# Performance work log

Measured on AMD Instinct MI355X. Metric: run time of the kernel, lower is better.

## Reference

```python
import jax, jax.numpy as jnp
import numpy as np

N, E, D, L = 100000, 600000, 128, 5
BN_EPS = 1e-5


def setup_inputs() -> dict:
    key = jax.random.key(0)
    ks = jax.random.split(key, 12)
    x = jax.random.normal(ks[0], (N, D), dtype=jnp.float32)
    edge_index = jax.random.randint(ks[1], (2, E), 0, N, dtype=jnp.int64)
    edge_attr = jax.random.randint(ks[2], (E, D), 0, 4, dtype=jnp.int32)
    # per-layer GCNConv params
    W = jax.random.normal(ks[3], (L, D, D), dtype=jnp.float32) * 0.05
    b = jax.random.normal(ks[4], (L, D), dtype=jnp.float32) * 0.01
    root = jax.random.normal(ks[5], (L, D), dtype=jnp.float32) * 0.05
    # BatchNorm1d eval-mode params / running stats
    gamma = 1.0 + 0.1 * jax.random.normal(ks[6], (L, D), dtype=jnp.float32)
    beta = 0.1 * jax.random.normal(ks[7], (L, D), dtype=jnp.float32)
    mean = 0.1 * jax.random.normal(ks[8], (L, D), dtype=jnp.float32)
    var = 0.5 + jax.random.uniform(ks[9], (L, D), dtype=jnp.float32)
    return {"x": x, "edge_index": edge_index, "edge_attr": edge_attr,
            "W": W, "b": b, "root": root,
            "gamma": gamma, "beta": beta, "mean": mean, "var": var}


def reference(x, edge_index, edge_attr, W, b, root, gamma, beta, mean, var):
    # edge_attr.long() then identity edge_encoder -> integer values used in float math
    e = edge_attr.astype(x.dtype)                      # [E, D]
    row, col = edge_index[0], edge_index[1]            # source j, target i
    # deg = degree(row) + 1 (same every layer since graph is fixed)
    deg = jax.ops.segment_sum(jnp.ones((E,), x.dtype), row, num_segments=N) + 1.0  # [N]
    dinv = deg ** -0.5
    norm = (dinv[row] * dinv[col])[:, None]            # [E, 1]
    h = x
    for l in range(L):
        hl = h @ W[l].T + b[l]                         # Linear(emb_dim, emb_dim)
        msg = norm * jax.nn.relu(hl[row] + e)          # gather + relu + scale  [E, D]
        agg = jax.ops.segment_sum(msg, col, num_segments=N)  # scatter-add at targets
        h = agg + jax.nn.relu(hl + root[l]) / deg[:, None]   # self-loop term
        # BatchNorm1d (eval mode, running stats)
        h = gamma[l] * (h - mean[l]) / jnp.sqrt(var[l] + BN_EPS) + beta[l]
        if l < L - 1:
            h = jax.nn.relu(h)                         # dropout is identity in eval
    return h  # JK='last'
```

## Files before the change

### kernel.cpp

```cpp
#include <hip/hip_runtime.h>
#include <cstdint>
#include <cstddef>

#define DF 128
#define NL 5
#define NB 1024
#define BN_EPS 1e-5f

typedef short bf16x8 __attribute__((ext_vector_type(8)));
typedef float f32x4 __attribute__((ext_vector_type(4)));

typedef __attribute__((address_space(3))) uint32_t lds_u32;
typedef __attribute__((address_space(1))) uint32_t glb_u32;

__device__ __forceinline__ void gload16(const void* g, void* l) {
#if __has_builtin(__builtin_amdgcn_global_load_lds)
  __builtin_amdgcn_global_load_lds((const glb_u32*)g, (lds_u32*)l, 16, 0, 0);
#else
  *(uint4*)l = *(const uint4*)g;
#endif
}

__device__ __forceinline__ ushort f2b(float f) {
  union { float f; uint32_t u; } v; v.f = f;
  uint32_t u = v.u + 0x7fffu + ((v.u >> 16) & 1u);
  return (ushort)(u >> 16);
}
__device__ __forceinline__ uint32_t pk2(float a, float b) {
  return (uint32_t)f2b(a) | ((uint32_t)f2b(b) << 16);
}
__device__ __forceinline__ float i8f(uint32_t w, int sh) {
  return (float)(int8_t)((w >> sh) & 0xffu);
}


__global__ void k_deg2(const int* __restrict__ row, const int* __restrict__ col,
                       int* __restrict__ degi, int* __restrict__ indeg, int E) {
  int i = blockIdx.x * blockDim.x + threadIdx.x;
  if (i < E) {
    atomicAdd(&degi[row[i]], 1);
    atomicAdd(&indeg[col[i]], 1);
  }
}

__global__ void k_dinvhist(const int* __restrict__ degi, const int* __restrict__ indeg,
                           float* __restrict__ dinv, int* __restrict__ hist, int N) {
  __shared__ int lh[NB];
  for (int j = threadIdx.x; j < NB; j += blockDim.x) lh[j] = 0;
  __syncthreads();
  int i = blockIdx.x * blockDim.x + threadIdx.x;
  if (i < N) {
    dinv[i] = 1.0f / sqrtf((float)(degi[i] + 1));
    atomicAdd(&lh[min(indeg[i], NB - 1)], 1);
  }
  __syncthreads();
  for (int j = threadIdx.x; j < NB; j += blockDim.x) {
    int c = lh[j];
    if (c) atomicAdd(&hist[j], c);
  }
}

__global__ void k_scan(const int* __restrict__ hist,
                       int* __restrict__ nodeStart, int* __restrict__ edgeStart) {
  __shared__ int2 sm[NB];
  int t = threadIdx.x;
  int c = hist[t];
  int2 v; v.x = c; v.y = c * t;
  sm[t] = v;
  __syncthreads();
  for (int off = 1; off < NB; off <<= 1) {
    int2 add; add.x = 0; add.y = 0;
    if (t >= off) add = sm[t - off];
    __syncthreads();
    sm[t].x += add.x; sm[t].y += add.y;
    __syncthreads();
  }
  nodeStart[t] = sm[t].x - c;
  edgeStart[t] = sm[t].y - c * t;
}

__global__ void k_assign(const int* __restrict__ indeg, const float* __restrict__ dinv,
                         const int* __restrict__ nodeStart, const int* __restrict__ edgeStart,
                         int* __restrict__ binCursor,
                         int* __restrict__ perm, int* __restrict__ invperm,
                         int* __restrict__ startP, int* __restrict__ cursorP,
                         int* __restrict__ degP, float* __restrict__ dinvP, int N) {
  __shared__ int lh[NB];
  __shared__ int gbase[NB];
  for (int j = threadIdx.x; j < NB; j += blockDim.x) lh[j] = 0;
  __syncthreads();
  int nd = blockIdx.x * blockDim.x + threadIdx.x;
  bool valid = nd < N;
  int d = 0, bin = 0, lrank = 0;
  if (valid) {
    d = indeg[nd];
    bin = min(d, NB - 1);
    lrank = atomicAdd(&lh[bin], 1);
  }
  __syncthreads();
  for (int j = threadIdx.x; j < NB; j += blockDim.x) {
    int c = lh[j];
    gbase[j] = c ? atomicAdd(&binCursor[j], c) : 0;
  }
  __syncthreads();
  if (!valid) return;
  int r = gbase[bin] + lrank;
  int i = nodeStart[bin] + r;
  perm[i] = nd;
  invperm[nd] = i;
  int st = edgeStart[bin] + r * d;
  startP[i] = st;
  cursorP[i] = st;
  degP[i] = d;
  dinvP[i] = dinv[nd];
}

__global__ void k_fillpack(const int* __restrict__ row, const int* __restrict__ col,
                           const float* __restrict__ dinv, const int* __restrict__ invperm,
                           int* __restrict__ cursorP, int2* __restrict__ pairS,
                           const int* __restrict__ ea, uint32_t* __restrict__ epS, int E) {
  int tid = blockIdx.x * blockDim.x + threadIdx.x;
  int e = tid >> 3, t = tid & 7;
  if (e >= E) return;
  int pos;
  if (t == 0) {
    int r = row[e], c = col[e];
    pos = atomicAdd(&cursorP[invperm[c]], 1);
    int2 pv; pv.x = invperm[r];
    float nr = dinv[r] * dinv[c];
    pv.y = __float_as_int(nr);
    pairS[pos] = pv;
  }
  pos = __shfl(pos, 0, 8);
  const int4* p = ((const int4*)ea) + (size_t)e * 32 + t * 4;
  uint32_t w = 0;
  #pragma unroll
  for (int q = 0; q < 4; ++q) {
    int4 a = p[q];
    w |= ((uint32_t)(a.x & 3)) << (8 * q);
    w |= ((uint32_t)(a.y & 3)) << (8 * q + 2);
    w |= ((uint32_t)(a.z & 3)) << (8 * q + 4);
    w |= ((uint32_t)(a.w & 3)) << (8 * q + 6);
  }
  epS[(size_t)pos * 8 + t] = w;
}

__global__ void k_params(const float* __restrict__ g, const float* __restrict__ be,
                         const float* __restrict__ mn, const float* __restrict__ vr,
                         float* __restrict__ s, float* __restrict__ t,
                         const float* __restrict__ W, ushort* __restrict__ Wb,
                         int nbn, int nw) {
  int i = blockIdx.x * blockDim.x + threadIdx.x;
  if (i < nw) Wb[i] = f2b(W[i]);
  if (i < nbn) {
    float sc = g[i] / sqrtf(vr[i] + BN_EPS);
    s[i] = sc;
    t[i] = be[i] - mn[i] * sc;
  }
}

template <typename IT>
__global__ __launch_bounds__(256) void k_gemm(
    const IT* __restrict__ in, const int* __restrict__ perm,
    const ushort* __restrict__ Wb, const float* __restrict__ bl,
    uint8_t* __restrict__ hl, float* __restrict__ scale, int N)
{
  __shared__ uint4 lA[128 * 16];
  __shared__ uint4 lW[128 * 16];
  const int t = threadIdx.x;
  const int row0 = blockIdx.x * 128;
  const int wv = t >> 6;
  const int l  = t & 63;

  #pragma unroll
  for (int it = 0; it < 8; ++it) {
    int ubase = (it * 4 + wv) * 64;
    int lin = ubase + l;
    int r = lin >> 4, u = lin & 15;
    gload16((const void*)((const uint4*)Wb + (r << 4) + (u ^ (r & 7))), (void*)(lW + ubase));
  }

  if constexpr (sizeof(IT) == 2) {
    #pragma unroll
    for (int it = 0; it < 8; ++it) {
      int ubase = (it * 4 + wv) * 64;
      int lin = ubase + l;
      int r = lin >> 4, u = lin & 15;
      int gn = row0 + r;
      int gnc = gn < N ? gn : N - 1;
      gload16((const void*)((const uint4*)in + (size_t)gnc * 16 + (u ^ (r & 7))),
              (void*)(lA + ubase));
    }
  } else {
    #pragma unroll
    for (int it = 0; it < 8; ++it) {
      int lin = it * 256 + t;
      int r = lin >> 4, u = lin & 15;
      int gn = row0 + r;
      uint4 pk = make_uint4(0u, 0u, 0u, 0u);
      if (gn < N) {
        int src = perm[gn];
        const float4* p = (const float4*)((const float*)in + (size_t)src * DF + u * 8);
        float4 f0 = p[0], f1 = p[1];
        pk.x = pk2(f0.x, f0.y); pk.y = pk2(f0.z, f0.w);
        pk.z = pk2(f1.x, f1.y); pk.w = pk2(f1.z, f1.w);
      }
      lA[(r << 4) | (u ^ (r & 7))] = pk;
    }
  }
  __syncthreads();

  const int lr = l & 15;
  const int lk = l >> 4;

  f32x4 acc[2][8];
  #pragma unroll
  for (int rt = 0; rt < 2; ++rt)
    #pragma unroll
    for (int ct = 0; ct < 8; ++ct) acc[rt][ct] = (f32x4){0.f, 0.f, 0.f, 0.f};

  #pragma unroll
  for (int ks = 0; ks < 4; ++ks) {
    const int kofs = ks * 4 + lk;
    bf16x8 af[2], wf[8];
    #pragma unroll
    for (int rt = 0; rt < 2; ++rt) {
      int r = wv * 32 + rt * 16 + lr;
      af[rt] = *reinterpret_cast<const bf16x8*>(&lA[(r << 4) | (kofs ^ (r & 7))]);
    }
    #pragma unroll
    for (int ct = 0; ct < 8; ++ct) {
      int r = ct * 16 + lr;
      wf[ct] = *reinterpret_cast<const bf16x8*>(&lW[(r << 4) | (kofs ^ (r & 7))]);
    }
    #pragma unroll
    for (int rt = 0; rt < 2; ++rt)
      #pragma unroll
      for (int ct = 0; ct < 8; ++ct)
        acc[rt][ct] = __builtin_amdgcn_mfma_f32_16x16x32_bf16(af[rt], wf[ct], acc[rt][ct], 0, 0, 0);
  }

  float bb[8];
  #pragma unroll
  for (int ct = 0; ct < 8; ++ct) bb[ct] = bl[ct * 16 + lr];

  __syncthreads();
  uint8_t* q8 = (uint8_t*)lA;

  #pragma unroll
  for (int rt = 0; rt < 2; ++rt) {
    #pragma unroll
    for (int rg = 0; rg < 4; ++rg) {
      int rloc = wv * 32 + rt * 16 + lk * 4 + rg;
      float o[8];
      float am = 0.f;
      #pragma unroll
      for (int ct = 0; ct < 8; ++ct) {
        o[ct] = acc[rt][ct][rg] + bb[ct];
        am = fmaxf(am, fabsf(o[ct]));
      }
      am = fmaxf(am, __shfl_xor(am, 1));
      am = fmaxf(am, __shfl_xor(am, 2));
      am = fmaxf(am, __shfl_xor(am, 4));
      am = fmaxf(am, __shfl_xor(am, 8));
      float inv = am > 0.f ? 127.f / am : 0.f;
      int gn = row0 + rloc;
      if (lr == 0 && gn < N) scale[gn] = am * (1.f / 127.f);
      #pragma unroll
      for (int ct = 0; ct < 8; ++ct) {
        int q = __float2int_rn(o[ct] * inv);
        q8[rloc * DF + ct * 16 + lr] = (uint8_t)(q & 0xff);
      }
    }
  }
  __syncthreads();

  #pragma unroll
  for (int it = 0; it < 8; ++it) {
    int chunk = it * 256 + t;
    int rloc = chunk >> 4;
    int gn = row0 + rloc;
    if (gn < N) {
      uint2 v = *(const uint2*)(q8 + chunk * 8);
      *(uint2*)(hl + (size_t)gn * DF + (chunk & 15) * 8) = v;
    }
  }
}

template <typename AT, bool LAST>
__global__ __launch_bounds__(256) void k_gather(
    const int* __restrict__ startP, const int* __restrict__ degP,
    const float* __restrict__ dinvP,
    const int2* __restrict__ pairS,
    const uint32_t* __restrict__ epS,
    const uint4* __restrict__ hl4, const float* __restrict__ scaleArr,
    const float* __restrict__ rootl, const float* __restrict__ sl,
    const float* __restrict__ tl, const int* __restrict__ perm,
    AT* __restrict__ acc, int N)
{
  int gw = (blockIdx.x * blockDim.x + threadIdx.x) >> 6;
  int lane = threadIdx.x & 63;
  int s8 = lane & 7;
  int i = gw * 8 + (lane >> 3);
  if (i >= N) return;
  int base = startP[i], n = degP[i];
  float di = dinvP[i];
  float invdeg = di * di;

  float a[16];
  #pragma unroll
  for (int j = 0; j < 16; ++j) a[j] = 0.f;

  for (int c0 = 0; c0 < n; c0 += 8) {
    int m = min(8, n - c0);
    int2 pv = (s8 < m) ? pairS[base + c0 + s8] : make_int2(0, 0);
    #pragma unroll 2
    for (int k = 0; k < m; ++k) {
      int src = __shfl(pv.x, k, 8);
      float nr = __int_as_float(__shfl(pv.y, k, 8));
      uint32_t pw = epS[(size_t)(base + c0 + k) * 8 + s8];
      uint4 hw = hl4[(size_t)src * 8 + s8];
      float sc = scaleArr[src];
      #pragma unroll
      for (int q = 0; q < 4; ++q) {
        uint32_t hword = q == 0 ? hw.x : (q == 1 ? hw.y : (q == 2 ? hw.z : hw.w));
        #pragma unroll
        for (int bj = 0; bj < 4; ++bj) {
          int j = q * 4 + bj;
          float ev = (float)((pw >> (2 * j)) & 3u);
          a[j] += nr * fmaxf(fmaf(i8f(hword, 8 * bj), sc, ev), 0.f);
        }
      }
    }
  }

  uint4 hwS = hl4[(size_t)i * 8 + s8];
  float scS = scaleArr[i];
  float hs[16];
  #pragma unroll
  for (int q = 0; q < 4; ++q) {
    uint32_t hword = q == 0 ? hwS.x : (q == 1 ? hwS.y : (q == 2 ? hwS.z : hwS.w));
    #pragma unroll
    for (int bj = 0; bj < 4; ++bj) hs[q * 4 + bj] = i8f(hword, 8 * bj) * scS;
  }

  float rr[16], ss[16], tt[16];
  #pragma unroll
  for (int q = 0; q < 4; ++q) {
    ((float4*)rr)[q] = ((const float4*)rootl)[s8 * 4 + q];
    ((float4*)ss)[q] = ((const float4*)sl)[s8 * 4 + q];
    ((float4*)tt)[q] = ((const float4*)tl)[s8 * 4 + q];
  }

  float o[16];
  #pragma unroll
  for (int j = 0; j < 16; ++j) {
    float self = fmaxf(hs[j] + rr[j], 0.f) * invdeg;
    o[j] = ss[j] * (self + a[j]) + tt[j];
  }

  if constexpr (!LAST) {
    #pragma unroll
    for (int j = 0; j < 16; ++j) o[j] = fmaxf(o[j], 0.f);
    uint4 p0, p1;
    p0.x = pk2(o[0], o[1]);   p0.y = pk2(o[2], o[3]);
    p0.z = pk2(o[4], o[5]);   p0.w = pk2(o[6], o[7]);
    p1.x = pk2(o[8], o[9]);   p1.y = pk2(o[10], o[11]);
    p1.z = pk2(o[12], o[13]); p1.w = pk2(o[14], o[15]);
    uint4* ap = (uint4*)acc + (size_t)i * 16 + s8 * 2;
    ap[0] = p0; ap[1] = p1;
  } else {
    int nd = perm[i];
    float4* ap = (float4*)acc + (size_t)nd * 32 + s8 * 4;
    ap[0] = make_float4(o[0], o[1], o[2], o[3]);
    ap[1] = make_float4(o[4], o[5], o[6], o[7]);
    ap[2] = make_float4(o[8], o[9], o[10], o[11]);
    ap[3] = make_float4(o[12], o[13], o[14], o[15]);
  }
}

extern "C" void kernel_launch(void* const* d_in, const int* in_sizes, int n_in,
                              void* d_out, int out_size, void* d_ws, size_t ws_size,
                              hipStream_t stream) {
  const float* x     = (const float*)d_in[0];
  const int*   ei    = (const int*)d_in[1];
  const int*   ea    = (const int*)d_in[2];
  const float* W     = (const float*)d_in[3];
  const float* b     = (const float*)d_in[4];
  const float* root  = (const float*)d_in[5];
  const float* gamma = (const float*)d_in[6];
  const float* beta  = (const float*)d_in[7];
  const float* mean  = (const float*)d_in[8];
  const float* var   = (const float*)d_in[9];

  const int N = in_sizes[0] / DF;
  const int E = in_sizes[1] / 2;
  const int* row = ei;
  const int* col = ei + E;

  char* ws = (char*)d_ws;
  size_t off = 0;
  auto alloc = [&](size_t bytes) -> void* {
    void* p = ws + off;
    off = (off + bytes + 255) & ~(size_t)255;
    return p;
  };
  int*      degi    = (int*)alloc((size_t)N * 4);
  int*      indeg   = (int*)alloc((size_t)N * 4);
  int*      hist    = (int*)alloc((size_t)NB * 4);
  int*      binCur  = (int*)alloc((size_t)NB * 4);
  size_t    zspan   = (size_t)((char*)ws + off - (char*)degi);
  float*    dinv    = (float*)alloc((size_t)N * 4);
  int*      nodeSt  = (int*)alloc((size_t)NB * 4);
  int*      edgeSt  = (int*)alloc((size_t)NB * 4);
  int*      perm    = (int*)alloc((size_t)N * 4);
  int*      invperm = (int*)alloc((size_t)N * 4);
  int*      startP  = (int*)alloc((size_t)N * 4);
  int*      cursorP = (int*)alloc((size_t)N * 4);
  int*      degP    = (int*)alloc((size_t)N * 4);
  float*    dinvP   = (float*)alloc((size_t)N * 4);
  int2*     pairS   = (int2*)alloc((size_t)E * 8);
  uint32_t* epS     = (uint32_t*)alloc((size_t)E * 8 * 4);
  float*    sbuf    = (float*)alloc((size_t)NL * DF * 4);
  float*    tbuf    = (float*)alloc((size_t)NL * DF * 4);
  ushort*   Wb      = (ushort*)alloc((size_t)NL * DF * DF * 2);
  uint8_t*  hl      = (uint8_t*)alloc((size_t)N * DF);
  float*    scaleA  = (float*)alloc((size_t)N * 4);
  ushort*   accP    = (ushort*)alloc((size_t)N * DF * 2);

  hipMemsetAsync(degi, 0, zspan, stream);

  k_deg2<<<(E + 255) / 256, 256, 0, stream>>>(row, col, degi, indeg, E);
  k_dinvhist<<<(N + 255) / 256, 256, 0, stream>>>(degi, indeg, dinv, hist, N);
  k_scan<<<1, NB, 0, stream>>>(hist, nodeSt, edgeSt);
  k_assign<<<(N + 255) / 256, 256, 0, stream>>>(indeg, dinv, nodeSt, edgeSt, binCur,
                                                perm, invperm, startP, cursorP,
                                                degP, dinvP, N);
  k_fillpack<<<(E * 8 + 255) / 256, 256, 0, stream>>>(row, col, dinv, invperm, cursorP,
                                                      pairS, ea, epS, E);
  k_params<<<(NL * DF * DF + 255) / 256, 256, 0, stream>>>(
      gamma, beta, mean, var, sbuf, tbuf, W, Wb, NL * DF, NL * DF * DF);

  float* outp = (float*)d_out;
  const int gemmGrid = (N + 127) / 128;
  const int gathGrid = (((N + 7) / 8) * 64 + 255) / 256;

  k_gemm<float><<<gemmGrid, 256, 0, stream>>>(x, perm, Wb, b, hl, scaleA, N);
  k_gather<ushort, false><<<gathGrid, 256, 0, stream>>>(
      startP, degP, dinvP, pairS, epS, (const uint4*)hl, scaleA,
      root, sbuf, tbuf, perm, accP, N);

  for (int l = 1; l < NL - 1; ++l) {
    k_gemm<ushort><<<gemmGrid, 256, 0, stream>>>(
        accP, nullptr, Wb + (size_t)l * DF * DF, b + (size_t)l * DF, hl, scaleA, N);
    k_gather<ushort, false><<<gathGrid, 256, 0, stream>>>(
        startP, degP, dinvP, pairS, epS, (const uint4*)hl, scaleA,
        root + (size_t)l * DF, sbuf + (size_t)l * DF, tbuf + (size_t)l * DF,
        perm, accP, N);
  }

  {
    const int l = NL - 1;
    k_gemm<ushort><<<gemmGrid, 256, 0, stream>>>(
        accP, nullptr, Wb + (size_t)l * DF * DF, b + (size_t)l * DF, hl, scaleA, N);
    k_gather<float, true><<<gathGrid, 256, 0, stream>>>(
        startP, degP, dinvP, pairS, epS, (const uint4*)hl, scaleA,
        root + (size_t)l * DF, sbuf + (size_t)l * DF, tbuf + (size_t)l * DF,
        perm, outp, N);
  }
}
```

Measured before the change: 411.1 us.

## Fuse gather-aggregate of layer l with next layer's GEMM in one kernel

Replaces the separate gather and GEMM kernels for the middle layers with one fused kernel. Each 512-thread block aggregates 128 nodes into LDS as bf16, then runs the MFMA GEMM with the next layer's weights and writes int8-quantised output with per-row scales. Ping-pong buffers hold the input and output activations. This removes the bf16 activation round trip through global memory and several launches, at the cost of serialising the irregular gather and the GEMM inside each block, which may lower occupancy and latency hiding.

After: 425.0 us. 1.03x slower.

```diff
diff --git a/kernel.cpp b/kernel.cpp
--- a/kernel.cpp
+++ b/kernel.cpp
@@ -159,9 +159,8 @@
   }
 }
 
-template <typename IT>
-__global__ __launch_bounds__(256) void k_gemm(
-    const IT* __restrict__ in, const int* __restrict__ perm,
+__global__ __launch_bounds__(256) void k_gemm0(
+    const float* __restrict__ in, const int* __restrict__ perm,
     const ushort* __restrict__ Wb, const float* __restrict__ bl,
     uint8_t* __restrict__ hl, float* __restrict__ scale, int N)
 {
@@ -179,34 +178,20 @@
     int r = lin >> 4, u = lin & 15;
     gload16((const void*)((const uint4*)Wb + (r << 4) + (u ^ (r & 7))), (void*)(lW + ubase));
   }
-
-  if constexpr (sizeof(IT) == 2) {
-    #pragma unroll
-    for (int it = 0; it < 8; ++it) {
-      int ubase = (it * 4 + wv) * 64;
-      int lin = ubase + l;
-      int r = lin >> 4, u = lin & 15;
-      int gn = row0 + r;
-      int gnc = gn < N ? gn : N - 1;
-      gload16((const void*)((const uint4*)in + (size_t)gnc * 16 + (u ^ (r & 7))),
-              (void*)(lA + ubase));
-    }
-  } else {
-    #pragma unroll
-    for (int it = 0; it < 8; ++it) {
-      int lin = it * 256 + t;
-      int r = lin >> 4, u = lin & 15;
-      int gn = row0 + r;
-      uint4 pk = make_uint4(0u, 0u, 0u, 0u);
-      if (gn < N) {
-        int src = perm[gn];
-        const float4* p = (const float4*)((const float*)in + (size_t)src * DF + u * 8);
-        float4 f0 = p[0], f1 = p[1];
-        pk.x = pk2(f0.x, f0.y); pk.y = pk2(f0.z, f0.w);
-        pk.z = pk2(f1.x, f1.y); pk.w = pk2(f1.z, f1.w);
-      }
-      lA[(r << 4) | (u ^ (r & 7))] = pk;
-    }
+  #pragma unroll
+  for (int it = 0; it < 8; ++it) {
+    int lin = it * 256 + t;
+    int r = lin >> 4, u = lin & 15;
+    int gn = row0 + r;
+    uint4 pk = make_uint4(0u, 0u, 0u, 0u);
+    if (gn < N) {
+      int src = perm[gn];
+      const float4* p = (const float4*)(in + (size_t)src * DF + u * 8);
+      float4 f0 = p[0], f1 = p[1];
+      pk.x = pk2(f0.x, f0.y); pk.y = pk2(f0.z, f0.w);
+      pk.z = pk2(f1.x, f1.y); pk.w = pk2(f1.z, f1.w);
+    }
+    lA[(r << 4) | (u ^ (r & 7))] = pk;
   }
   __syncthreads();
 
@@ -287,8 +272,177 @@
   }
 }
 
-template <typename AT, bool LAST>
-__global__ __launch_bounds__(256) void k_gather(
+__global__ __launch_bounds__(512, 4) void k_fused(
+    const int* __restrict__ startP, const int* __restrict__ degP,
+    const float* __restrict__ dinvP,
+    const int2* __restrict__ pairS, const uint32_t* __restrict__ epS,
+    const uint4* __restrict__ hlIn, const float* __restrict__ scaleIn,
+    const float* __restrict__ rootl, const float* __restrict__ sl,
+    const float* __restrict__ tl,
+    const ushort* __restrict__ Wb, const float* __restrict__ bl,
+    uint8_t* __restrict__ hlOut, float* __restrict__ scaleOut, int N)
+{
+  __shared__ uint4 lA[128 * 16];
+  __shared__ uint4 lW[128 * 16];
+  const int t = threadIdx.x;
+  const int row0 = blockIdx.x * 128;
+  const int wv = t >> 6;
+  const int l  = t & 63;
+
+  #pragma unroll
+  for (int it = 0; it < 4; ++it) {
+    int ubase = (it * 8 + wv) * 64;
+    int lin = ubase + l;
+    int r = lin >> 4, u = lin & 15;
+    gload16((const void*)((const uint4*)Wb + (r << 4) + (u ^ (r & 7))), (void*)(lW + ubase));
+  }
+
+  const int s8 = t & 7;
+  const int nib = t >> 3;
+  #pragma unroll
+  for (int pass = 0; pass < 2; ++pass) {
+    int r = pass * 64 + nib;
+    int i = row0 + r;
+    float o[16];
+    if (i < N) {
+      int base = startP[i], n = degP[i];
+      float di = dinvP[i];
+      float invdeg = di * di;
+      float a[16];
+      #pragma unroll
+      for (int j = 0; j < 16; ++j) a[j] = 0.f;
+
+      for (int c0 = 0; c0 < n; c0 += 8) {
+        int m = min(8, n - c0);
+        int2 pv = (s8 < m) ? pairS[base + c0 + s8] : make_int2(0, 0);
+        #pragma unroll 2
+        for (int k = 0; k < m; ++k) {
+          int src = __shfl(pv.x, k, 8);
+          float nr = __int_as_float(__shfl(pv.y, k, 8));
+          uint32_t pw = epS[(size_t)(base + c0 + k) * 8 + s8];
+          uint4 hw = hlIn[(size_t)src * 8 + s8];
+          float sc = scaleIn[src];
+          #pragma unroll
+          for (int q = 0; q < 4; ++q) {
+            uint32_t hword = q == 0 ? hw.x : (q == 1 ? hw.y : (q == 2 ? hw.z : hw.w));
+            #pragma unroll
+            for (int bj = 0; bj < 4; ++bj) {
+              int j = q * 4 + bj;
+              float ev = (float)((pw >> (2 * j)) & 3u);
+              a[j] += nr * fmaxf(fmaf(i8f(hword, 8 * bj), sc, ev), 0.f);
+            }
+          }
+        }
+      }
+
+      uint4 hwS = hlIn[(size_t)i * 8 + s8];
+      float scS = scaleIn[i];
+      float hs[16];
+      #pragma unroll
+      for (int q = 0; q < 4; ++q) {
+        uint32_t hword = q == 0 ? hwS.x : (q == 1 ? hwS.y : (q == 2 ? hwS.z : hwS.w));
+        #pragma unroll
+        for (int bj = 0; bj < 4; ++bj) hs[q * 4 + bj] = i8f(hword, 8 * bj) * scS;
+      }
+
+      float rr[16], ss[16], tt[16];
+      #pragma unroll
+      for (int q = 0; q < 4; ++q) {
+        ((float4*)rr)[q] = ((const float4*)rootl)[s8 * 4 + q];
+        ((float4*)ss)[q] = ((const float4*)sl)[s8 * 4 + q];
+        ((float4*)tt)[q] = ((const float4*)tl)[s8 * 4 + q];
+      }
+      #pragma unroll
+      for (int j = 0; j < 16; ++j) {
+        float self = fmaxf(hs[j] + rr[j], 0.f) * invdeg;
+        o[j] = fmaxf(ss[j] * (self + a[j]) + tt[j], 0.f);
+      }
+    } else {
+      #pragma unroll
+      for (int j = 0; j < 16; ++j) o[j] = 0.f;
+    }
+
+    uint4 p0, p1;
+    p0.x = pk2(o[0], o[1]);   p0.y = pk2(o[2], o[3]);
+    p0.z = pk2(o[4], o[5]);   p0.w = pk2(o[6], o[7]);
+    p1.x = pk2(o[8], o[9]);   p1.y = pk2(o[10], o[11]);
+    p1.z = pk2(o[12], o[13]); p1.w = pk2(o[14], o[15]);
+    int u0 = 2 * s8, u1 = 2 * s8 + 1;
+    lA[(r << 4) | (u0 ^ (r & 7))] = p0;
+    lA[(r << 4) | (u1 ^ (r & 7))] = p1;
+  }
+  __syncthreads();
+
+  const int lr = l & 15;
+  const int lk = l >> 4;
+
+  f32x4 acc[8];
+  #pragma unroll
+  for (int ct = 0; ct < 8; ++ct) acc[ct] = (f32x4){0.f, 0.f, 0.f, 0.f};
+
+  #pragma unroll
+  for (int ks = 0; ks < 4; ++ks) {
+    const int kofs = ks * 4 + lk;
+    bf16x8 af, wf[8];
+    {
+      int r = wv * 16 + lr;
+      af = *reinterpret_cast<const bf16x8*>(&lA[(r << 4) | (kofs ^ (r & 7))]);
+    }
+    #pragma unroll
+    for (int ct = 0; ct < 8; ++ct) {
+      int r = ct * 16 + lr;
+      wf[ct] = *reinterpret_cast<const bf16x8*>(&lW[(r << 4) | (kofs ^ (r & 7))]);
+    }
+    #pragma unroll
+    for (int ct = 0; ct < 8; ++ct)
+      acc[ct] = __builtin_amdgcn_mfma_f32_16x16x32_bf16(af, wf[ct], acc[ct], 0, 0, 0);
+  }
+
+  float bb[8];
+  #pragma unroll
+  for (int ct = 0; ct < 8; ++ct) bb[ct] = bl[ct * 16 + lr];
+
+  __syncthreads();
+  uint8_t* q8 = (uint8_t*)lA;
+
+  #pragma unroll
+  for (int rg = 0; rg < 4; ++rg) {
+    int rloc = wv * 16 + lk * 4 + rg;
+    float o[8];
+    float am = 0.f;
+    #pragma unroll
+    for (int ct = 0; ct < 8; ++ct) {
+      o[ct] = acc[ct][rg] + bb[ct];
+      am = fmaxf(am, fabsf(o[ct]));
+    }
+    am = fmaxf(am, __shfl_xor(am, 1));
+    am = fmaxf(am, __shfl_xor(am, 2));
+    am = fmaxf(am, __shfl_xor(am, 4));
+    am = fmaxf(am, __shfl_xor(am, 8));
+    float inv = am > 0.f ? 127.f / am : 0.f;
+    int gn = row0 + rloc;
+    if (lr == 0 && gn < N) scaleOut[gn] = am * (1.f / 127.f);
+    #pragma unroll
+    for (int ct = 0; ct < 8; ++ct) {
+      int q = __float2int_rn(o[ct] * inv);
+      q8[rloc * DF + ct * 16 + lr] = (uint8_t)(q & 0xff);
+    }
+  }
+  __syncthreads();
+
+  #pragma unroll
+  for (int it = 0; it < 4; ++it) {
+    int chunk = it * 512 + t;
+    int rloc = chunk >> 4;
+    int gn = row0 + rloc;
+    if (gn < N) {
+      uint2 v = *(const uint2*)(q8 + chunk * 8);
+      *(uint2*)(hlOut + (size_t)gn * DF + (chunk & 15) * 8) = v;
+    }
+  }
+}
+
+__global__ __launch_bounds__(256) void k_gather_last(
     const int* __restrict__ startP, const int* __restrict__ degP,
     const float* __restrict__ dinvP,
     const int2* __restrict__ pairS,
@@ -296,7 +450,7 @@
     const uint4* __restrict__ hl4, const float* __restrict__ scaleArr,
     const float* __restrict__ rootl, const float* __restrict__ sl,
     const float* __restrict__ tl, const int* __restrict__ perm,
-    AT* __restrict__ acc, int N)
+    float* __restrict__ acc, int N)
 {
   int gw = (blockIdx.x * blockDim.x + threadIdx.x) >> 6;
   int lane = threadIdx.x & 63;
@@ -359,24 +513,12 @@
     o[j] = ss[j] * (self + a[j]) + tt[j];
   }
 
-  if constexpr (!LAST) {
-    #pragma unroll
-    for (int j = 0; j < 16; ++j) o[j] = fmaxf(o[j], 0.f);
-    uint4 p0, p1;
-    p0.x = pk2(o[0], o[1]);   p0.y = pk2(o[2], o[3]);
-    p0.z = pk2(o[4], o[5]);   p0.w = pk2(o[6], o[7]);
-    p1.x = pk2(o[8], o[9]);   p1.y = pk2(o[10], o[11]);
-    p1.z = pk2(o[12], o[13]); p1.w = pk2(o[14], o[15]);
-    uint4* ap = (uint4*)acc + (size_t)i * 16 + s8 * 2;
-    ap[0] = p0; ap[1] = p1;
-  } else {
-    int nd = perm[i];
-    float4* ap = (float4*)acc + (size_t)nd * 32 + s8 * 4;
-    ap[0] = make_float4(o[0], o[1], o[2], o[3]);
-    ap[1] = make_float4(o[4], o[5], o[6], o[7]);
-    ap[2] = make_float4(o[8], o[9], o[10], o[11]);
-    ap[3] = make_float4(o[12], o[13], o[14], o[15]);
-  }
+  int nd = perm[i];
+  float4* ap = (float4*)acc + (size_t)nd * 32 + s8 * 4;
+  ap[0] = make_float4(o[0], o[1], o[2], o[3]);
+  ap[1] = make_float4(o[4], o[5], o[6], o[7]);
+  ap[2] = make_float4(o[8], o[9], o[10], o[11]);
+  ap[3] = make_float4(o[12], o[13], o[14], o[15]);
 }
 
 extern "C" void kernel_launch(void* const* d_in, const int* in_sizes, int n_in,
@@ -424,9 +566,10 @@
   float*    sbuf    = (float*)alloc((size_t)NL * DF * 4);
   float*    tbuf    = (float*)alloc((size_t)NL * DF * 4);
   ushort*   Wb      = (ushort*)alloc((size_t)NL * DF * DF * 2);
-  uint8_t*  hl      = (uint8_t*)alloc((size_t)N * DF);
-  float*    scaleA  = (float*)alloc((size_t)N * 4);
-  ushort*   accP    = (ushort*)alloc((size_t)N * DF * 2);
+  uint8_t*  hlA     = (uint8_t*)alloc((size_t)N * DF);
+  uint8_t*  hlB     = (uint8_t*)alloc((size_t)N * DF);
+  float*    scA     = (float*)alloc((size_t)N * 4);
+  float*    scB     = (float*)alloc((size_t)N * 4);
 
   hipMemsetAsync(degi, 0, zspan, stream);
 
@@ -442,29 +585,27 @@
       gamma, beta, mean, var, sbuf, tbuf, W, Wb, NL * DF, NL * DF * DF);
 
   float* outp = (float*)d_out;
-  const int gemmGrid = (N + 127) / 128;
-  const int gathGrid = (((N + 7) / 8) * 64 + 255) / 256;
-
-  k_gemm<float><<<gemmGrid, 256, 0, stream>>>(x, perm, Wb, b, hl, scaleA, N);
-  k_gather<ushort, false><<<gathGrid, 256, 0, stream>>>(
-      startP, degP, dinvP, pairS, epS, (const uint4*)hl, scaleA,
-      root, sbuf, tbuf, perm, accP, N);
-
-  for (int l = 1; l < NL - 1; ++l) {
-    k_gemm<ushort><<<gemmGrid, 256, 0, stream>>>(
-        accP, nullptr, Wb + (size_t)l * DF * DF, b + (size_t)l * DF, hl, scaleA, N);
-    k_gather<ushort, false><<<gathGrid, 256, 0, stream>>>(
-        startP, degP, dinvP, pairS, epS, (const uint4*)hl, scaleA,
+  const int tiles = (N + 127) / 128;
+
+  k_gemm0<<<tiles, 256, 0, stream>>>(x, perm, Wb, b, hlA, scA, N);
+
+  uint8_t* hin = hlA; float* sin_ = scA;
+  uint8_t* hout = hlB; float* sout = scB;
+  for (int l = 0; l < NL - 1; ++l) {
+    k_fused<<<tiles, 512, 0, stream>>>(
+        startP, degP, dinvP, pairS, epS,
+        (const uint4*)hin, sin_,
         root + (size_t)l * DF, sbuf + (size_t)l * DF, tbuf + (size_t)l * DF,
-        perm, accP, N);
+        Wb + (size_t)(l + 1) * DF * DF, b + (size_t)(l + 1) * DF,
+        hout, sout, N);
+    uint8_t* th = hin; hin = hout; hout = th;
+    float* ts = sin_; sin_ = sout; sout = ts;
   }
 
   {
     const int l = NL - 1;
-    k_gemm<ushort><<<gemmGrid, 256, 0, stream>>>(
-        accP, nullptr, Wb + (size_t)l * DF * DF, b + (size_t)l * DF, hl, scaleA, N);
-    k_gather<float, true><<<gathGrid, 256, 0, stream>>>(
-        startP, degP, dinvP, pairS, epS, (const uint4*)hl, scaleA,
+    k_gather_last<<<(((N + 7) / 8) * 64 + 255) / 256, 256, 0, stream>>>(
+        startP, degP, dinvP, pairS, epS, (const uint4*)hin, sin_,
         root + (size_t)l * DF, sbuf + (size_t)l * DF, tbuf + (size_t)l * DF,
         perm, outp, N);
   }
```
